# Optimization experiments

Measured on AMD Instinct MI355X. Metric: run time of the kernel, lower is better.

Reference implementation:

```python
import jax, jax.numpy as jnp
import numpy as np

B = 8192          # batch of independent BFGS problems
TX = 16           # transmit antennas
N = 2 * TX        # real-valued problem size
ITER = 10         # outer BFGS iterations
RO = 0.5          # backtracking shrink factor
C = 1e-4          # Armijo constant
MAX_BT = 25       # fixed unroll of the data-dependent backtracking loop (0.5**25 ~ 3e-8)


def setup_inputs() -> dict:
    key = jax.random.key(0)
    k1, k2, k3 = jax.random.split(key, 3)
    h = jax.random.normal(k1, (B, N, N), jnp.float32) / np.float32(np.sqrt(N))
    x_true = jax.random.normal(k2, (B, N), jnp.float32)
    # y = h @ x_true + noise : realistic, well-posed least-squares instances
    y = jnp.einsum('bij,bj->bi', h, x_true) + 0.1 * jax.random.normal(k3, (B, N), jnp.float32)
    x = jnp.zeros((B, N), jnp.float32)
    alpha = jnp.ones((B,), jnp.float32)
    h_k = jnp.broadcast_to(jnp.eye(N, dtype=jnp.float32), (B, N, N))  # BFGS identity init
    return {"y": y, "h": h, "x": x, "alpha": alpha, "h_k": h_k, "iteration": ITER}


def _bfgs(y, h, x, alpha, h_k, iteration):
    y = y[..., None]          # [B, N, 1]
    x = x[..., None]          # [B, N, 1]
    hT = jnp.swapaxes(h, 1, 2)

    def f_value(pt):                      # [B, 1]
        return jnp.linalg.norm(y - h @ pt, axis=1) / 2

    def grad_value(pt):                   # [B, N, 1]
        return hT @ (h @ pt) - hT @ y

    for _ in range(iteration):
        g = grad_value(x)
        p = -(h_k @ g)                    # search direction [B, N, 1]
        fx = f_value(x)                   # [B, 1]
        gp = (jnp.swapaxes(g, 1, 2) @ p)[:, :, 0]   # g^T p, [B, 1]
        # Armijo backtracking: fixed unroll of `while any(...): alpha = where(..., ro*alpha, alpha)`
        for _ in range(MAX_BT):
            lhs = f_value(x + alpha[:, None, None] * p)[:, 0]        # [B]
            rhs = (fx + C * alpha[:, None] * gp)[:, 0]               # [B]
            alpha = jnp.where(lhs > rhs, RO * alpha, alpha)
        x_new = x + alpha[:, None, None] * p
        s = x_new - x
        y_k = grad_value(x_new) - g
        sT = jnp.swapaxes(s, 1, 2)
        ykT = jnp.swapaxes(y_k, 1, 2)
        auxSc = sT @ y_k                  # [B, 1, 1]
        h_k = (h_k
               + (auxSc + ykT @ (h_k @ y_k)) * (s @ sT) / auxSc ** 2
               - ((h_k @ (y_k @ sT)) + s @ (ykT @ h_k)) / auxSc)
        x = x_new
    return x[:, :, 0]


def reference(y, h, x, alpha, h_k, iteration):
    return _bfgs(y, h, x, alpha, h_k, iteration)
```

## Files before the change

kernel.cpp:

```cpp
#include <hip/hip_runtime.h>
#include <math.h>


__device__ __forceinline__ float rlane63(float v) {
    return __int_as_float(__builtin_amdgcn_readlane(__float_as_int(v), 63));
}

template <int CTRL>
__device__ __forceinline__ float dpp_mov(float v) {
    return __int_as_float(
        __builtin_amdgcn_update_dpp(0, __float_as_int(v), CTRL, 0xf, 0xf, true));
}
template <int CTRL>
__device__ __forceinline__ float dppadd(float v) { return v + dpp_mov<CTRL>(v); }

__device__ __forceinline__ float wavesum(float v) {
    v = dppadd<0xB1>(v);
    v = dppadd<0x4E>(v);
    v = dppadd<0x141>(v);
    v = dppadd<0x140>(v);
    v = dppadd<0x142>(v);
    v = dppadd<0x143>(v);
    return rlane63(v);
}


#define ROT_FMA_BLOCK(M, V, A0, A1)                                        \
    asm volatile(                                                          \
        "s_nop 1\n\t"                                                      \
        "v_mul_f32 %0, %2, %3\n\t"                                         \
        "v_mul_f32_dpp %1, %3, %4 row_ror:15 row_mask:0xf bank_mask:0xf bound_ctrl:1\n\t" \
        "v_fmac_f32_dpp %0, %3, %5 row_ror:14 row_mask:0xf bank_mask:0xf bound_ctrl:1\n\t" \
        "v_fmac_f32_dpp %1, %3, %6 row_ror:13 row_mask:0xf bank_mask:0xf bound_ctrl:1\n\t" \
        "v_fmac_f32_dpp %0, %3, %7 row_ror:12 row_mask:0xf bank_mask:0xf bound_ctrl:1\n\t" \
        "v_fmac_f32_dpp %1, %3, %8 row_ror:11 row_mask:0xf bank_mask:0xf bound_ctrl:1\n\t" \
        "v_fmac_f32_dpp %0, %3, %9 row_ror:10 row_mask:0xf bank_mask:0xf bound_ctrl:1\n\t" \
        "v_fmac_f32_dpp %1, %3, %10 row_ror:9 row_mask:0xf bank_mask:0xf bound_ctrl:1\n\t" \
        "v_fmac_f32_dpp %0, %3, %11 row_ror:8 row_mask:0xf bank_mask:0xf bound_ctrl:1\n\t" \
        "v_fmac_f32_dpp %1, %3, %12 row_ror:7 row_mask:0xf bank_mask:0xf bound_ctrl:1\n\t" \
        "v_fmac_f32_dpp %0, %3, %13 row_ror:6 row_mask:0xf bank_mask:0xf bound_ctrl:1\n\t" \
        "v_fmac_f32_dpp %1, %3, %14 row_ror:5 row_mask:0xf bank_mask:0xf bound_ctrl:1\n\t" \
        "v_fmac_f32_dpp %0, %3, %15 row_ror:4 row_mask:0xf bank_mask:0xf bound_ctrl:1\n\t" \
        "v_fmac_f32_dpp %1, %3, %16 row_ror:3 row_mask:0xf bank_mask:0xf bound_ctrl:1\n\t" \
        "v_fmac_f32_dpp %0, %3, %17 row_ror:2 row_mask:0xf bank_mask:0xf bound_ctrl:1\n\t" \
        "v_fmac_f32_dpp %1, %3, %18 row_ror:1 row_mask:0xf bank_mask:0xf bound_ctrl:1\n\t" \
        : "=&v"(A0), "=&v"(A1)                                             \
        : "v"((M)[0]), "v"(V), "v"((M)[1]), "v"((M)[2]), "v"((M)[3]),      \
          "v"((M)[4]), "v"((M)[5]), "v"((M)[6]), "v"((M)[7]), "v"((M)[8]), \
          "v"((M)[9]), "v"((M)[10]), "v"((M)[11]), "v"((M)[12]),           \
          "v"((M)[13]), "v"((M)[14]), "v"((M)[15]))

__device__ __forceinline__ float fwd_mv(const float (&M)[16], float v) {
    float a0, a1;
    ROT_FMA_BLOCK(M, v, a0, a1);
    const float acc = a0 + a1;
    return acc + __shfl_xor(acc, 32);
}

__device__ __forceinline__ float trp_mv(const float (&M)[16], float u) {
    float a0, a1;
    ROT_FMA_BLOCK(M, u, a0, a1);
    const float acc = a0 + a1;
    return acc + __shfl_xor(acc, 16);
}

__device__ __forceinline__ float relayout(float x, bool mid) {
    const float sw = __shfl_xor(x, 48);
    return mid ? sw : x;
}

#define LPAD 33

__global__ __launch_bounds__(256) void bfgs_kernel(
    const float* __restrict__ y_g,
    const float* __restrict__ h_g,
    const int*   __restrict__ iter_g,
    float*       __restrict__ out)
{
    __shared__ __align__(16) float Hs[4][32 * LPAD];

    const int tid  = threadIdx.x;
    const int l    = tid & 63;
    const int w    = tid >> 6;
    const int prob = blockIdx.x * 4 + w;

    const int  i   = l & 15;
    const int  a   = l >> 4;
    const int  c   = l >> 5;
    const int  r   = a & 1;
    const bool mid = (a == 1) || (a == 2);

    const float* __restrict__ hb = h_g + (size_t)prob * 1024;
    float* Hp = Hs[w];

    #pragma unroll
    for (int u = 0; u < 4; ++u) {
        const int f = u * 256 + l * 4;
        const float4 v4 = *reinterpret_cast<const float4*>(hb + f);
        const int r0 = f >> 5, c0 = f & 31;
        float* d = Hp + r0 * LPAD + c0;
        d[0] = v4.x; d[1] = v4.y; d[2] = v4.z; d[3] = v4.w;
    }
    __builtin_amdgcn_wave_barrier();

    float Hr[16], Ht[16];
    const int rbase = (16 * r + i) * LPAD + 16 * c;
    #pragma unroll
    for (int k = 0; k < 16; ++k) {
        const int ik = (i + k) & 15;
        Hr[k] = Hp[rbase + ik];
        Ht[k] = Hp[(16 * r + ik) * LPAD + 16 * c + i];
    }

    float hkr[16];
    #pragma unroll
    for (int k = 0; k < 16; ++k) hkr[k] = 0.f;
    hkr[0] = (r == c) ? 1.f : 0.f;

    const float yq = y_g[prob * 32 + 16 * r + i];
    float g  = -trp_mv(Ht, yq);
    float rr = 0.5f * wavesum(yq * yq);

    float p_v = -g;
    float p_q = relayout(p_v, mid);
    float gp  = -0.5f * wavesum(g * g);

    float x = 0.f, alpha = 1.f;
    const int niter = iter_g[0];

    for (int it = 0; it < niter; ++it) {
        const float u_q = fwd_mv(Hr, p_v);
        const float qq  = 0.5f * wavesum(u_q * u_q);
        const float t   = trp_mv(Ht, u_q);

        const float rq  = -gp;
        const float fx  = 0.5f * sqrtf(rr);
        const float a_c = ldexpf(alpha, -(l & 31));
        const float rhs = fx + (1e-4f * a_c) * gp;
        const float phi = fmaf(a_c, fmaf(a_c, qq, -2.f * rq), rr);
        const bool cond = (rhs < 0.f) || (0.25f * phi > rhs * rhs);
        const unsigned long long bal = __ballot(cond);
        const unsigned mh  = (unsigned)bal;
        const unsigned inv = (~mh & 0x01FFFFFFu) | 0x02000000u;
        alpha = ldexpf(alpha, -(__ffs(inv) - 1));

        x = fmaf(alpha, p_v, x);
        rr = fmaf(alpha, fmaf(alpha, qq, -2.f * rq), rr);

        const float s   = alpha * p_v;
        const float s_q = alpha * p_q;
        const float aux = (alpha * alpha) * qq;

        const float yk = alpha * t;
        g += yk;

        const float ht_q = fwd_mv(hkr, t);
        const float htv  = relayout(ht_q, mid);
        const float yhy  = 0.5f * wavesum(yk * (alpha * htv));

        const float hy_q = alpha * ht_q;
        const float inva = 1.f / aux;
        const float c1   = (aux + yhy) * (inva * inva);
        const float uR   = fmaf(c1, s_q, -(hy_q * inva));
        const float wR   = -(s_q * inva) * alpha;

        asm volatile(
            "s_nop 1\n\t"
            "v_fmac_f32 %0, %16, %18\n\t"
            "v_fmac_f32 %0, %17, %19\n\t"
            "v_fmac_f32_dpp %1, %16, %18 row_ror:15 row_mask:0xf bank_mask:0xf bound_ctrl:1\n\t"
            "v_fmac_f32_dpp %1, %17, %19 row_ror:15 row_mask:0xf bank_mask:0xf bound_ctrl:1\n\t"
            "v_fmac_f32_dpp %2, %16, %18 row_ror:14 row_mask:0xf bank_mask:0xf bound_ctrl:1\n\t"
            "v_fmac_f32_dpp %2, %17, %19 row_ror:14 row_mask:0xf bank_mask:0xf bound_ctrl:1\n\t"
            "v_fmac_f32_dpp %3, %16, %18 row_ror:13 row_mask:0xf bank_mask:0xf bound_ctrl:1\n\t"
            "v_fmac_f32_dpp %3, %17, %19 row_ror:13 row_mask:0xf bank_mask:0xf bound_ctrl:1\n\t"
            "v_fmac_f32_dpp %4, %16, %18 row_ror:12 row_mask:0xf bank_mask:0xf bound_ctrl:1\n\t"
            "v_fmac_f32_dpp %4, %17, %19 row_ror:12 row_mask:0xf bank_mask:0xf bound_ctrl:1\n\t"
            "v_fmac_f32_dpp %5, %16, %18 row_ror:11 row_mask:0xf bank_mask:0xf bound_ctrl:1\n\t"
            "v_fmac_f32_dpp %5, %17, %19 row_ror:11 row_mask:0xf bank_mask:0xf bound_ctrl:1\n\t"
            "v_fmac_f32_dpp %6, %16, %18 row_ror:10 row_mask:0xf bank_mask:0xf bound_ctrl:1\n\t"
            "v_fmac_f32_dpp %6, %17, %19 row_ror:10 row_mask:0xf bank_mask:0xf bound_ctrl:1\n\t"
            "v_fmac_f32_dpp %7, %16, %18 row_ror:9 row_mask:0xf bank_mask:0xf bound_ctrl:1\n\t"
            "v_fmac_f32_dpp %7, %17, %19 row_ror:9 row_mask:0xf bank_mask:0xf bound_ctrl:1\n\t"
            "v_fmac_f32_dpp %8, %16, %18 row_ror:8 row_mask:0xf bank_mask:0xf bound_ctrl:1\n\t"
            "v_fmac_f32_dpp %8, %17, %19 row_ror:8 row_mask:0xf bank_mask:0xf bound_ctrl:1\n\t"
            "v_fmac_f32_dpp %9, %16, %18 row_ror:7 row_mask:0xf bank_mask:0xf bound_ctrl:1\n\t"
            "v_fmac_f32_dpp %9, %17, %19 row_ror:7 row_mask:0xf bank_mask:0xf bound_ctrl:1\n\t"
            "v_fmac_f32_dpp %10, %16, %18 row_ror:6 row_mask:0xf bank_mask:0xf bound_ctrl:1\n\t"
            "v_fmac_f32_dpp %10, %17, %19 row_ror:6 row_mask:0xf bank_mask:0xf bound_ctrl:1\n\t"
            "v_fmac_f32_dpp %11, %16, %18 row_ror:5 row_mask:0xf bank_mask:0xf bound_ctrl:1\n\t"
            "v_fmac_f32_dpp %11, %17, %19 row_ror:5 row_mask:0xf bank_mask:0xf bound_ctrl:1\n\t"
            "v_fmac_f32_dpp %12, %16, %18 row_ror:4 row_mask:0xf bank_mask:0xf bound_ctrl:1\n\t"
            "v_fmac_f32_dpp %12, %17, %19 row_ror:4 row_mask:0xf bank_mask:0xf bound_ctrl:1\n\t"
            "v_fmac_f32_dpp %13, %16, %18 row_ror:3 row_mask:0xf bank_mask:0xf bound_ctrl:1\n\t"
            "v_fmac_f32_dpp %13, %17, %19 row_ror:3 row_mask:0xf bank_mask:0xf bound_ctrl:1\n\t"
            "v_fmac_f32_dpp %14, %16, %18 row_ror:2 row_mask:0xf bank_mask:0xf bound_ctrl:1\n\t"
            "v_fmac_f32_dpp %14, %17, %19 row_ror:2 row_mask:0xf bank_mask:0xf bound_ctrl:1\n\t"
            "v_fmac_f32_dpp %15, %16, %18 row_ror:1 row_mask:0xf bank_mask:0xf bound_ctrl:1\n\t"
            "v_fmac_f32_dpp %15, %17, %19 row_ror:1 row_mask:0xf bank_mask:0xf bound_ctrl:1\n\t"
            : "+v"(hkr[0]), "+v"(hkr[1]), "+v"(hkr[2]), "+v"(hkr[3]),
              "+v"(hkr[4]), "+v"(hkr[5]), "+v"(hkr[6]), "+v"(hkr[7]),
              "+v"(hkr[8]), "+v"(hkr[9]), "+v"(hkr[10]), "+v"(hkr[11]),
              "+v"(hkr[12]), "+v"(hkr[13]), "+v"(hkr[14]), "+v"(hkr[15])
            : "v"(s), "v"(htv), "v"(uR), "v"(wR));

        const float ia  = 1.f / alpha;
        const float k1  = fmaf(alpha, gp, aux);
        const float k2  = fmaf(yhy, ia, -qq);
        p_q = fmaf(-alpha, ht_q, p_q);
        p_q = fmaf(-k1, uR, p_q);
        p_q = fmaf(-k2, wR, p_q);
        p_v = relayout(p_q, mid);
        gp  = gp + alpha * qq - alpha * k2
            - c1 * k1 * k1 + 2.f * (inva * alpha) * k1 * k2;
    }

    if (r == 0) out[prob * 32 + 16 * c + i] = x;
}

extern "C" void kernel_launch(void* const* d_in, const int* in_sizes, int n_in,
                              void* d_out, int out_size, void* d_ws, size_t ws_size,
                              hipStream_t stream) {
    const float* y  = (const float*)d_in[0];
    const float* hh = (const float*)d_in[1];
    const int*   it = (const int*)d_in[5];
    float* out = (float*)d_out;

    const int B = in_sizes[0] / 32;
    dim3 grid(B / 4), block(256);
    bfgs_kernel<<<grid, block, 0, stream>>>(y, hh, it, out);
}
```

Before: 34.85 us.

## Precompute Gram matrix H^T H with split-bf16 MFMA to halve per-iteration matvecs

Forms G = H^T H once per problem using MFMA 32x32x16 bf16 instructions on a hi/lo bf16 split, which recovers near-fp32 accuracy. Each BFGS iteration then does one matvec with G in place of a forward plus a transposed matvec with H. The curvature term qq becomes p^T G p. This adds a one-time setup cost of eight MFMAs plus an LDS round trip. The lo*lo terms and bf16 rounding may add small numerical error.

```diff
diff --git a/kernel.cpp b/kernel.cpp
--- a/kernel.cpp
+++ b/kernel.cpp
@@ -69,6 +69,17 @@
     return mid ? sw : x;
 }
 
+__device__ __forceinline__ unsigned short f2bf(float x) {
+    unsigned u = __float_as_uint(x);
+    return (unsigned short)((u + 0x7FFFu + ((u >> 16) & 1u)) >> 16);
+}
+__device__ __forceinline__ float bf2f(unsigned short h) {
+    return __uint_as_float(((unsigned)h) << 16);
+}
+
+typedef float f32x16 __attribute__((ext_vector_type(16)));
+typedef short s16x8  __attribute__((ext_vector_type(8)));
+
 #define LPAD 33
 
 __global__ __launch_bounds__(256) void bfgs_kernel(
@@ -103,23 +114,58 @@
     }
     __builtin_amdgcn_wave_barrier();
 
-    float Hr[16], Ht[16];
+    const float yq = y_g[prob * 32 + 16 * r + i];
+    float g;
+    {
+        float Htt[16];
+        #pragma unroll
+        for (int k = 0; k < 16; ++k) {
+            const int ik = (i + k) & 15;
+            Htt[k] = Hp[(16 * r + ik) * LPAD + 16 * c + i];
+        }
+        g = -trp_mv(Htt, yq);
+    }
+    float rr = 0.5f * wavesum(yq * yq);
+
+    s16x8 hi0, lo0, hi1, lo1;
+    #pragma unroll
+    for (int j = 0; j < 8; ++j) {
+        const int m = 8 * (l >> 5) + j;
+        const float v0 = Hp[m * LPAD + (l & 31)];
+        const float v1 = Hp[(m + 16) * LPAD + (l & 31)];
+        const unsigned short h0 = f2bf(v0);
+        const unsigned short h1 = f2bf(v1);
+        hi0[j] = (short)h0; lo0[j] = (short)f2bf(v0 - bf2f(h0));
+        hi1[j] = (short)h1; lo1[j] = (short)f2bf(v1 - bf2f(h1));
+    }
+    f32x16 acc = {};
+    acc = __builtin_amdgcn_mfma_f32_32x32x16_bf16(lo0, lo0, acc, 0, 0, 0);
+    acc = __builtin_amdgcn_mfma_f32_32x32x16_bf16(lo1, lo1, acc, 0, 0, 0);
+    acc = __builtin_amdgcn_mfma_f32_32x32x16_bf16(hi0, lo0, acc, 0, 0, 0);
+    acc = __builtin_amdgcn_mfma_f32_32x32x16_bf16(lo0, hi0, acc, 0, 0, 0);
+    acc = __builtin_amdgcn_mfma_f32_32x32x16_bf16(hi1, lo1, acc, 0, 0, 0);
+    acc = __builtin_amdgcn_mfma_f32_32x32x16_bf16(lo1, hi1, acc, 0, 0, 0);
+    acc = __builtin_amdgcn_mfma_f32_32x32x16_bf16(hi0, hi0, acc, 0, 0, 0);
+    acc = __builtin_amdgcn_mfma_f32_32x32x16_bf16(hi1, hi1, acc, 0, 0, 0);
+    __builtin_amdgcn_wave_barrier();
+
+    #pragma unroll
+    for (int reg = 0; reg < 16; ++reg) {
+        const int row = (reg & 3) + 8 * (reg >> 2) + 4 * (l >> 5);
+        Hp[row * LPAD + (l & 31)] = acc[reg];
+    }
+    __builtin_amdgcn_wave_barrier();
+
+    float Gr[16];
     const int rbase = (16 * r + i) * LPAD + 16 * c;
     #pragma unroll
-    for (int k = 0; k < 16; ++k) {
-        const int ik = (i + k) & 15;
-        Hr[k] = Hp[rbase + ik];
-        Ht[k] = Hp[(16 * r + ik) * LPAD + 16 * c + i];
-    }
+    for (int k = 0; k < 16; ++k)
+        Gr[k] = Hp[rbase + ((i + k) & 15)];
 
     float hkr[16];
     #pragma unroll
     for (int k = 0; k < 16; ++k) hkr[k] = 0.f;
     hkr[0] = (r == c) ? 1.f : 0.f;
-
-    const float yq = y_g[prob * 32 + 16 * r + i];
-    float g  = -trp_mv(Ht, yq);
-    float rr = 0.5f * wavesum(yq * yq);
 
     float p_v = -g;
     float p_q = relayout(p_v, mid);
@@ -129,9 +175,9 @@
     const int niter = iter_g[0];
 
     for (int it = 0; it < niter; ++it) {
-        const float u_q = fwd_mv(Hr, p_v);
-        const float qq  = 0.5f * wavesum(u_q * u_q);
-        const float t   = trp_mv(Ht, u_q);
+        const float t_q = fwd_mv(Gr, p_v);
+        const float qq  = 0.5f * wavesum(p_q * t_q);
+        const float t_v = relayout(t_q, mid);
 
         const float rq  = -gp;
         const float fx  = 0.5f * sqrtf(rr);
@@ -150,11 +196,10 @@
         const float s   = alpha * p_v;
         const float s_q = alpha * p_q;
         const float aux = (alpha * alpha) * qq;
-
-        const float yk = alpha * t;
+        const float yk  = alpha * t_v;
         g += yk;
 
-        const float ht_q = fwd_mv(hkr, t);
+        const float ht_q = fwd_mv(hkr, t_v);
         const float htv  = relayout(ht_q, mid);
         const float yhy  = 0.5f * wavesum(yk * (alpha * htv));
 
```

After: 33.93 us (median of 2 runs). 1.03x faster.
